# Optimization experiments

Measured on AMD Instinct MI355X. Metric: run time of the kernel, lower is better.

## Reference

```python
import math
import jax, jax.numpy as jnp
import numpy as np
from jax import lax

B = 8
IN_CH = 512
OUT_CH = 256
K = 3
LATENT = 512
BLUR = [1, 3, 3, 1]
FACTOR = 2
H = W = 64
# p = len(blur) - factor - (K-1) = 0 -> pad = ((p+1)//2 + factor - 1, p//2 + 1) = (1, 1)
PAD0, PAD1 = 1, 1


def _make_blur_kernel():
    k = jnp.array(BLUR, jnp.float32)
    k = k[None, :] * k[:, None]          # separable -> 2D
    k = k / jnp.sum(k)
    return k * (FACTOR ** 2)             # make_kernel(blur, factor) scales by factor^2


def setup_inputs() -> dict:
    key = jax.random.key(0)
    k1, k2, k3, k4 = jax.random.split(key, 4)
    inputs = {
        "input": jax.random.normal(k1, (B, IN_CH, H, W), jnp.float32),
        "w": jax.random.normal(k2, (B, LATENT), jnp.float32),
        # learned params
        "affine_weight": jax.random.normal(k3, (IN_CH, LATENT), jnp.float32),
        "affine_bias": jnp.ones((IN_CH,), jnp.float32),  # bias_init=1
        "conv_weight": jax.random.normal(k4, (1, OUT_CH, IN_CH, K, K), jnp.float32),
    }
    return inputs


def reference(input, w, affine_weight, affine_bias, conv_weight):
    batch = input.shape[0]
    # EqualLinear: scale = 1/sqrt(latent_dim), lr_mul=1
    style = w @ (affine_weight * (1.0 / math.sqrt(LATENT))).T + affine_bias  # (B, IN_CH)
    # modulate
    scale = 1.0 / math.sqrt(IN_CH * K * K)
    weight = (scale * conv_weight) * style[:, None, :, None, None]          # (B, OUT, IN, K, K)
    # demodulate over (in, kh, kw)
    demod = lax.rsqrt(jnp.sum(weight * weight, axis=(2, 3, 4)) + 1e-8)      # (B, OUT)
    weight = weight * demod[:, :, None, None, None]
    # grouped conv_transpose2d (groups=batch, stride=2, pad=0) == per-sample
    # conv with lhs_dilation=2, spatial padding K-1, kernel spatially flipped.
    kflip = jnp.flip(weight, (-2, -1))                                      # (B, OUT, IN, K, K) OIHW

    def ct(x, kern):  # x: (IN, H, W), kern: (OUT, IN, K, K)
        return lax.conv_general_dilated(
            x[None], kern, window_strides=(1, 1),
            padding=[(K - 1, K - 1), (K - 1, K - 1)],
            lhs_dilation=(2, 2),
            dimension_numbers=("NCHW", "OIHW", "NCHW"))[0]

    out = jax.vmap(ct)(input, kflip)                                        # (B, OUT, 2H-2+K, 2W-2+K)
    # upfirdn2d with up=down=1: pad then depthwise correlate with flipped FIR kernel
    blur = jnp.flip(_make_blur_kernel())                                    # (4, 4)
    out = jnp.pad(out, ((0, 0), (0, 0), (PAD0, PAD1), (PAD0, PAD1)))
    dw = jnp.tile(blur[None, None], (OUT_CH, 1, 1, 1))                      # (OUT, 1, 4, 4)
    out = lax.conv_general_dilated(
        out, dw, window_strides=(1, 1), padding="VALID",
        feature_group_count=OUT_CH,
        dimension_numbers=("NCHW", "OIHW", "NCHW"))
    return out  # (B, OUT, 2H, 2W)
```

## Files before the change

### kernel.cpp

```cpp
#include <hip/hip_runtime.h>
#include <hip/hip_bf16.h>
#include <math.h>

#define NB 8
#define INCH 512
#define OUTCH 256
#define SP 4096
#define LAT 512
#define NTAP 9
#define MDIM (NTAP*OUTCH)

#define INV_SQRT_LAT 0.044194173824159216f
#define WSCALE 0.014731391274719738f

typedef __bf16 bf16x8 __attribute__((ext_vector_type(8)));
typedef float  f32x4  __attribute__((ext_vector_type(4)));

__device__ __forceinline__ unsigned short f2bf(float f) {
  unsigned u = __float_as_uint(f);
  u += 0x7fffu + ((u >> 16) & 1u);
  return (unsigned short)(u >> 16);
}
__device__ __forceinline__ float bf2f(unsigned short v) {
  return __uint_as_float((unsigned)v << 16);
}

__global__ void prep_k(const float* __restrict__ w, const float* __restrict__ aff,
                       const float* __restrict__ bias, float* __restrict__ style,
                       const float* __restrict__ cw, float* __restrict__ S,
                       unsigned short* __restrict__ w9) {
  if (blockIdx.x < 16) {
    int gid = blockIdx.x * 256 + threadIdx.x;
    int b = gid >> 9, i = gid & 511;
    const float4* wv = (const float4*)(w + (size_t)b * LAT);
    const float4* av = (const float4*)(aff + (size_t)i * LAT);
    float s = 0.f;
#pragma unroll 4
    for (int l = 0; l < LAT / 4; ++l) {
      float4 a = av[l], ww = wv[l];
      s += a.x * ww.x + a.y * ww.y + a.z * ww.z + a.w * ww.w;
    }
    style[gid] = s * INV_SQRT_LAT + bias[i];
  } else {
    int gid = (blockIdx.x - 16) * 256 + threadIdx.x;
    int o = gid >> 9, i = gid & 511;
    const float* p = cw + (size_t)gid * 9;
    float ss = 0.f, v[9];
#pragma unroll
    for (int t = 0; t < 9; ++t) { v[t] = p[t]; ss += v[t] * v[t]; }
    S[gid] = ss * (WSCALE * WSCALE);
#pragma unroll
    for (int t = 0; t < 9; ++t)
      w9[((size_t)(t * OUTCH + o)) * INCH + i] = f2bf(v[t] * WSCALE);
  }
}

__global__ void demod_k(const float* __restrict__ style, const float* __restrict__ S,
                        float* __restrict__ dmod) {
  int gid = blockIdx.x * 256 + threadIdx.x;
  int b = gid >> 8, o = gid & 255;
  const float4* sv = (const float4*)(style + (size_t)b * INCH);
  const float4* Sv = (const float4*)(S + (size_t)o * INCH);
  float acc = 0.f;
#pragma unroll 4
  for (int l = 0; l < INCH / 4; ++l) {
    float4 st = sv[l], s2 = Sv[l];
    acc += st.x * st.x * s2.x + st.y * st.y * s2.y + st.z * st.z * s2.z + st.w * st.w * s2.w;
  }
  dmod[gid] = 1.0f / sqrtf(acc + 1e-8f);
}

__global__ void modx_k(const float* __restrict__ x, const float* __restrict__ style,
                       unsigned short* __restrict__ xmt) {
  __shared__ float tile[32][33];
  int b = blockIdx.z;
  int s0 = blockIdx.x * 32;
  int i0 = blockIdx.y * 32;
  int c = threadIdx.x & 31, r = threadIdx.x >> 5;
#pragma unroll
  for (int p = 0; p < 4; ++p) {
    int ii = r + p * 8;
    tile[ii][c] = x[((size_t)(b * INCH + i0 + ii)) * SP + s0 + c] * style[b * INCH + i0 + ii];
  }
  __syncthreads();
#pragma unroll
  for (int p = 0; p < 4; ++p) {
    int ss = r + p * 8;
    xmt[((size_t)(b * SP + s0 + ss)) * INCH + i0 + c] = f2bf(tile[c][ss]);
  }
}

__global__ __launch_bounds__(512, 2)
void gemm_k(const unsigned short* __restrict__ A,
            const unsigned short* __restrict__ Bm,
            unsigned short* __restrict__ C) {
  __shared__ __align__(16) unsigned short lds[73728];
  Bm += (size_t)blockIdx.z * SP * INCH;
  C  += (size_t)blockIdx.z * MDIM * SP;
  const int tid  = threadIdx.x;
  const int lane = tid & 63;
  const int wid  = tid >> 6;
  const int wm   = (wid >> 1) * 64;
  const int wn   = (wid & 1) * 64;
  const int m0 = blockIdx.y * 256;
  const int n0 = blockIdx.x * 128;
  const int r16  = lane & 15;
  const int quad = lane >> 4;

  const int srow = tid >> 3;
  const int sgch = ((tid & 7) ^ (srow & 7)) * 8;
  const int swb  = wid * 512;

  f32x4 acc[4][4];
#pragma unroll
  for (int i = 0; i < 4; ++i)
#pragma unroll
    for (int j = 0; j < 4; ++j) acc[i][j] = (f32x4){0.f, 0.f, 0.f, 0.f};

#define STAGE_A2(T, IT0) do {                                                       \
    unsigned short* _la = &lds[(((T) % 3) * 16384) + swb];                          \
    const unsigned short* _ga = A + (size_t)(m0 + srow) * INCH + (T) * 64 + sgch;   \
    _Pragma("unroll")                                                               \
    for (int _it = (IT0); _it < (IT0) + 2; ++_it)                                   \
      __builtin_amdgcn_global_load_lds(                                             \
          (const __attribute__((address_space(1))) void*)(_ga + (size_t)_it * 64 * INCH), \
          (__attribute__((address_space(3))) void*)(_la + _it * 4096), 16, 0, 0);   \
  } while (0)

#define STAGE_B1(T, IT) do {                                                        \
    unsigned short* _lb = &lds[49152 + (((T) % 3) * 8192) + swb];                   \
    const unsigned short* _gb = Bm + (size_t)(n0 + (IT) * 64 + srow) * INCH + (T) * 64 + sgch; \
    __builtin_amdgcn_global_load_lds(                                               \
        (const __attribute__((address_space(1))) void*)_gb,                         \
        (__attribute__((address_space(3))) void*)(_lb + (IT) * 4096), 16, 0, 0);    \
  } while (0)

#define READ_A(MH) do {                                                             \
    _Pragma("unroll")                                                               \
    for (int _i = 0; _i < 2; ++_i) {                                                \
      const int _ra = wm + ((MH) * 2 + _i) * 16 + r16;                              \
      af[0][_i] = *(const bf16x8*)&As_[_ra * 64 + (((0 + quad) ^ (_ra & 7)) * 8)];  \
      af[1][_i] = *(const bf16x8*)&As_[_ra * 64 + (((4 + quad) ^ (_ra & 7)) * 8)];  \
    }                                                                               \
  } while (0)

#define READ_B(NH) do {                                                             \
    _Pragma("unroll")                                                               \
    for (int _j = 0; _j < 2; ++_j) {                                                \
      const int _rb = wn + ((NH) * 2 + _j) * 16 + r16;                              \
      bfv[0][_j] = *(const bf16x8*)&Bs_[_rb * 64 + (((0 + quad) ^ (_rb & 7)) * 8)]; \
      bfv[1][_j] = *(const bf16x8*)&Bs_[_rb * 64 + (((4 + quad) ^ (_rb & 7)) * 8)]; \
    }                                                                               \
  } while (0)

#define MFMA_Q(MH, NH) do {                                                         \
    __builtin_amdgcn_s_setprio(1);                                                  \
    _Pragma("unroll")                                                               \
    for (int _kk = 0; _kk < 2; ++_kk)                                               \
    _Pragma("unroll")                                                               \
    for (int _i = 0; _i < 2; ++_i)                                                  \
    _Pragma("unroll")                                                               \
    for (int _j = 0; _j < 2; ++_j)                                                  \
      acc[(MH)*2+_i][(NH)*2+_j] = __builtin_amdgcn_mfma_f32_16x16x32_bf16(          \
          af[_kk][_i], bfv[_kk][_j], acc[(MH)*2+_i][(NH)*2+_j], 0, 0, 0);           \
    __builtin_amdgcn_s_setprio(0);                                                  \
  } while (0)

  STAGE_A2(0, 0); STAGE_A2(0, 2); STAGE_B1(0, 0); STAGE_B1(0, 1);
  STAGE_A2(1, 0); STAGE_A2(1, 2); STAGE_B1(1, 0); STAGE_B1(1, 1);
  asm volatile("s_waitcnt vmcnt(6)" ::: "memory");
  __builtin_amdgcn_sched_barrier(0);
  __builtin_amdgcn_s_barrier();

  for (int t = 0; t < 8; ++t) {
    const unsigned short* As_ = &lds[(t % 3) * 16384];
    const unsigned short* Bs_ = &lds[49152 + (t % 3) * 8192];
    const bool st = (t < 6);
    bf16x8 af[2][2], bfv[2][2];
    if (st) STAGE_A2(t + 2, 0);
    READ_A(0); READ_B(0);
    __builtin_amdgcn_s_barrier();
    MFMA_Q(0, 0);
    __builtin_amdgcn_s_barrier();
    if (st) STAGE_A2(t + 2, 2);
    READ_B(1);
    __builtin_amdgcn_s_barrier();
    MFMA_Q(0, 1);
    __builtin_amdgcn_s_barrier();
    if (st) STAGE_B1(t + 2, 0);
    READ_A(1);
    __builtin_amdgcn_s_barrier();
    MFMA_Q(1, 1);
    __builtin_amdgcn_s_barrier();
    if (st) STAGE_B1(t + 2, 1);
    READ_B(0);
    __builtin_amdgcn_s_barrier();
    MFMA_Q(1, 0);
    if (t < 6) {
      asm volatile("s_waitcnt vmcnt(6)" ::: "memory");
      __builtin_amdgcn_sched_barrier(0);
    } else if (t == 6) {
      asm volatile("s_waitcnt vmcnt(0)" ::: "memory");
      __builtin_amdgcn_sched_barrier(0);
    }
    __builtin_amdgcn_s_barrier();
  }
#undef STAGE_A2
#undef STAGE_B1
#undef READ_A
#undef READ_B
#undef MFMA_Q

#pragma unroll
  for (int i = 0; i < 4; ++i)
#pragma unroll
    for (int j = 0; j < 4; ++j)
#pragma unroll
      for (int r = 0; r < 4; ++r) {
        int row = wm + i * 16 + quad * 4 + r;
        int col = wn + j * 16 + r16;
        int pc  = (col >> 3) ^ (row & 15);
        lds[row * 128 + pc * 8 + (col & 7)] = f2bf(acc[i][j][r]);
      }
  __syncthreads();
#pragma unroll
  for (int rr = 0; rr < 8; ++rr) {
    int row = rr * 32 + (tid >> 4);
    int c   = tid & 15;
    int pc  = c ^ (row & 15);
    uint4 v = *(const uint4*)&lds[row * 128 + pc * 8];
    *(uint4*)&C[(size_t)(m0 + row) * SP + n0 + c * 8] = v;
  }
}

#define STRIP 8
#define TLSTR 70
#define TLROWS 10
__global__ __launch_bounds__(256)
void combine_k(const unsigned short* __restrict__ T, const float* __restrict__ dm,
               float* __restrict__ out) {
  __shared__ __align__(16) unsigned short TlB[9 * TLROWS * TLSTR + 4];
  __shared__ __align__(16) float V[3 * TLROWS * 128];
  T   += (size_t)blockIdx.z * MDIM * SP;
  dm  += (size_t)blockIdx.z * OUTCH;
  out += (size_t)blockIdx.z * OUTCH * 128 * 128;
  const int o  = blockIdx.y;
  const int Y0 = blockIdx.x * STRIP;
  const int tid = threadIdx.x;

  {
    uint4* tz = (uint4*)TlB;
#pragma unroll
    for (int idx = tid; idx < 788; idx += 256) tz[idx] = (uint4){0u, 0u, 0u, 0u};
  }
  __syncthreads();

  for (int idx = tid; idx < 1440; idx += 256) {
    int tap = idx / 160;
    int rem = idx - tap * 160;
    int ry  = rem >> 4;
    int c16 = rem & 15;
    int Yg = Y0 - 1 + ry;
    if ((unsigned)Yg < 64u) {
      ushort4 v4 = *(const ushort4*)(T + (size_t)(tap * OUTCH + o) * SP + Yg * 64 + c16 * 4);
      unsigned short* dst = &TlB[(tap * TLROWS + ry) * TLSTR + 4 + c16 * 4];
      *(ushort2*)(dst)     = make_ushort2(v4.x, v4.y);
      *(ushort2*)(dst + 2) = make_ushort2(v4.z, v4.w);
    }
  }
  __syncthreads();

  {
    const int r  = tid >> 3;
    const int xc = tid & 7;
    if (r < 30) {
      const int c  = r / 10;
      const int yr = r - c * 10;
      const int X0 = xc * 8;
      float td[3][12];
#pragma unroll
      for (int d = 0; d < 3; ++d) {
        const unsigned short* src = &TlB[((c * 3 + d) * TLROWS + yr) * TLSTR + 2 + X0];
#pragma unroll
        for (int k = 0; k < 6; ++k) {
          ushort2 u2 = *(const ushort2*)(src + 2 * k);
          td[d][2 * k]     = bf2f(u2.x);
          td[d][2 * k + 1] = bf2f(u2.y);
        }
      }
      float vout[16];
#pragma unroll
      for (int Xl = 0; Xl < 8; ++Xl) {
        float a0 = td[0][Xl + 1], a1 = td[0][Xl + 2], a2 = td[0][Xl + 3];
        float b0 = td[1][Xl + 1], b1 = td[1][Xl + 2], b2 = td[1][Xl + 3];
        float c0 = td[2][Xl + 1], c1 = td[2][Xl + 2], c2 = td[2][Xl + 3];
        vout[2 * Xl]     = b0 + 3.f * c0 + 3.f * a1 + 3.f * b1 + c1 + a2;
        vout[2 * Xl + 1] = c0 + a1 + 3.f * b1 + 3.f * c1 + 3.f * a2 + b2;
      }
      float* vr = &V[(c * TLROWS + yr) * 128];
#pragma unroll
      for (int j = 0; j < 4; ++j) {
        int l = 4 * xc + j;
        int p = (l & ~3) | ((l & 3) ^ ((l >> 3) & 3));
        *(f32x4*)(vr + p * 4) = (f32x4){vout[4 * j], vout[4 * j + 1], vout[4 * j + 2], vout[4 * j + 3]};
      }
    }
  }
  __syncthreads();

  {
    const int y  = tid >> 4;
    const int py = y & 1;
    const int Yl = y >> 1;
    const float dmv = dm[o] * (1.0f / 16.0f);
    float* orow = out + ((size_t)o * 128 + (Y0 * 2 + y)) * 128;
#pragma unroll
    for (int xg = 0; xg < 2; ++xg) {
      int l = (tid & 15) + 16 * xg;
      int p = (l & ~3) | ((l & 3) ^ ((l >> 3) & 3));
      int off = p * 4;
      f32x4 v00 = *(const f32x4*)&V[((0 * TLROWS) + Yl + 0) * 128 + off];
      f32x4 v01 = *(const f32x4*)&V[((0 * TLROWS) + Yl + 1) * 128 + off];
      f32x4 v02 = *(const f32x4*)&V[((0 * TLROWS) + Yl + 2) * 128 + off];
      f32x4 v10 = *(const f32x4*)&V[((1 * TLROWS) + Yl + 0) * 128 + off];
      f32x4 v11 = *(const f32x4*)&V[((1 * TLROWS) + Yl + 1) * 128 + off];
      f32x4 v12 = *(const f32x4*)&V[((1 * TLROWS) + Yl + 2) * 128 + off];
      f32x4 v20 = *(const f32x4*)&V[((2 * TLROWS) + Yl + 0) * 128 + off];
      f32x4 v21 = *(const f32x4*)&V[((2 * TLROWS) + Yl + 1) * 128 + off];
      f32x4 v22 = *(const f32x4*)&V[((2 * TLROWS) + Yl + 2) * 128 + off];
      f32x4 r;
      if (py == 0)
        r = v10 + 3.f * v20 + 3.f * v01 + 3.f * v11 + v21 + v02;
      else
        r = v20 + v01 + 3.f * v11 + 3.f * v21 + 3.f * v02 + v12;
      r *= dmv;
      *(f32x4*)(orow + l * 4) = r;
    }
  }
}

extern "C" void kernel_launch(void* const* d_in, const int* in_sizes, int n_in,
                              void* d_out, int out_size, void* d_ws, size_t ws_size,
                              hipStream_t stream) {
  const float* x    = (const float*)d_in[0];
  const float* w    = (const float*)d_in[1];
  const float* aff  = (const float*)d_in[2];
  const float* bias = (const float*)d_in[3];
  const float* cw   = (const float*)d_in[4];
  float* out = (float*)d_out;
  char* ws = (char*)d_ws;
  float* style        = (float*)(ws);
  float* S            = (float*)(ws + 16384);
  float* dmod         = (float*)(ws + 540672);
  unsigned short* w9  = (unsigned short*)(ws + 548864);
  unsigned short* xmt = (unsigned short*)(ws + 2908160);
  unsigned short* T   = (unsigned short*)(ws + 36462592);

  hipLaunchKernelGGL(prep_k, dim3(528), dim3(256), 0, stream, w, aff, bias, style, cw, S, w9);
  hipLaunchKernelGGL(demod_k, dim3(8), dim3(256), 0, stream, style, S, dmod);
  hipLaunchKernelGGL(modx_k, dim3(128, 16, 8), dim3(256), 0, stream, x, style, xmt);
  hipLaunchKernelGGL(gemm_k, dim3(32, 9, NB), dim3(512), 0, stream, w9, xmt, T);
  hipLaunchKernelGGL(combine_k, dim3(64 / STRIP, 256, NB), dim3(256), 0, stream, T, dmod, out);
}
```

Measured before the change: 396.4 us.

## Parallelize demod reduction, vectorize modx stores, and double combine strip height

The demod kernel now gives each (batch, out-channel) pair 16 threads that reduce with shuffles, so the launch grows from 8 blocks to 128 and no longer leaves most of the GPU idle. The transposed bf16 stores in modx are grouped into 8-byte ushort4 writes instead of scalar 2-byte writes. The combine kernel handles 16 rows per block instead of 8, which lowers halo reloads and block count. The cost is more LDS per combine block, which could reduce occupancy.

After: 385.2 us. 2.8% less time.

```diff
diff --git a/kernel.cpp b/kernel.cpp
--- a/kernel.cpp
+++ b/kernel.cpp
@@ -57,17 +57,20 @@
 
 __global__ void demod_k(const float* __restrict__ style, const float* __restrict__ S,
                         float* __restrict__ dmod) {
-  int gid = blockIdx.x * 256 + threadIdx.x;
-  int b = gid >> 8, o = gid & 255;
-  const float4* sv = (const float4*)(style + (size_t)b * INCH);
-  const float4* Sv = (const float4*)(S + (size_t)o * INCH);
+  int g = blockIdx.x * 16 + (threadIdx.x >> 4);
+  int j = threadIdx.x & 15;
+  int b = g >> 8, o = g & 255;
+  const float4* sv = (const float4*)(style + (size_t)b * INCH + j * 32);
+  const float4* Sv = (const float4*)(S + (size_t)o * INCH + j * 32);
   float acc = 0.f;
-#pragma unroll 4
-  for (int l = 0; l < INCH / 4; ++l) {
+#pragma unroll
+  for (int l = 0; l < 8; ++l) {
     float4 st = sv[l], s2 = Sv[l];
     acc += st.x * st.x * s2.x + st.y * st.y * s2.y + st.z * st.z * s2.z + st.w * st.w * s2.w;
   }
-  dmod[gid] = 1.0f / sqrtf(acc + 1e-8f);
+#pragma unroll
+  for (int d = 1; d < 16; d <<= 1) acc += __shfl_xor(acc, d, 16);
+  if (j == 0) dmod[g] = 1.0f / sqrtf(acc + 1e-8f);
 }
 
 __global__ void modx_k(const float* __restrict__ x, const float* __restrict__ style,
@@ -83,10 +86,15 @@
     tile[ii][c] = x[((size_t)(b * INCH + i0 + ii)) * SP + s0 + c] * style[b * INCH + i0 + ii];
   }
   __syncthreads();
-#pragma unroll
-  for (int p = 0; p < 4; ++p) {
-    int ss = r + p * 8;
-    xmt[((size_t)(b * SP + s0 + ss)) * INCH + i0 + c] = f2bf(tile[c][ss]);
+  {
+    int ss = threadIdx.x >> 3;
+    int c4 = threadIdx.x & 7;
+    ushort4 v;
+    v.x = f2bf(tile[c4 * 4 + 0][ss]);
+    v.y = f2bf(tile[c4 * 4 + 1][ss]);
+    v.z = f2bf(tile[c4 * 4 + 2][ss]);
+    v.w = f2bf(tile[c4 * 4 + 3][ss]);
+    *(ushort4*)&xmt[((size_t)(b * SP + s0 + ss)) * INCH + i0 + c4 * 4] = v;
   }
 }
 
@@ -233,9 +241,9 @@
   }
 }
 
-#define STRIP 8
+#define STRIP 16
 #define TLSTR 70
-#define TLROWS 10
+#define TLROWS 18
 __global__ __launch_bounds__(256)
 void combine_k(const unsigned short* __restrict__ T, const float* __restrict__ dm,
                float* __restrict__ out) {
@@ -250,76 +258,77 @@
 
   {
     uint4* tz = (uint4*)TlB;
-#pragma unroll
-    for (int idx = tid; idx < 788; idx += 256) tz[idx] = (uint4){0u, 0u, 0u, 0u};
-  }
-  __syncthreads();
-
-  for (int idx = tid; idx < 1440; idx += 256) {
-    int tap = idx / 160;
-    int rem = idx - tap * 160;
-    int ry  = rem >> 4;
-    int c16 = rem & 15;
-    int Yg = Y0 - 1 + ry;
+    for (int idx = tid; idx < (9 * TLROWS * TLSTR + 4) / 8; idx += 256)
+      tz[idx] = (uint4){0u, 0u, 0u, 0u};
+  }
+  __syncthreads();
+
+  for (int idx = tid; idx < 9 * TLROWS * 8; idx += 256) {
+    int tap = idx / (TLROWS * 8);
+    int rem = idx - tap * (TLROWS * 8);
+    int ry  = rem >> 3;
+    int c8  = rem & 7;
+    int Yg  = Y0 - 1 + ry;
     if ((unsigned)Yg < 64u) {
-      ushort4 v4 = *(const ushort4*)(T + (size_t)(tap * OUTCH + o) * SP + Yg * 64 + c16 * 4);
-      unsigned short* dst = &TlB[(tap * TLROWS + ry) * TLSTR + 4 + c16 * 4];
-      *(ushort2*)(dst)     = make_ushort2(v4.x, v4.y);
-      *(ushort2*)(dst + 2) = make_ushort2(v4.z, v4.w);
+      const unsigned short* src = T + (size_t)(tap * OUTCH + o) * SP + Yg * 64 + c8 * 8;
+      ushort4 a  = *(const ushort4*)(src);
+      ushort4 b4 = *(const ushort4*)(src + 4);
+      unsigned short* dst = &TlB[(tap * TLROWS + ry) * TLSTR + 4 + c8 * 8];
+      *(ushort2*)(dst)     = make_ushort2(a.x, a.y);
+      *(ushort2*)(dst + 2) = make_ushort2(a.z, a.w);
+      *(ushort2*)(dst + 4) = make_ushort2(b4.x, b4.y);
+      *(ushort2*)(dst + 6) = make_ushort2(b4.z, b4.w);
+    }
+  }
+  __syncthreads();
+
+  for (int idx = tid; idx < 3 * TLROWS * 8; idx += 256) {
+    const int r  = idx >> 3;
+    const int xc = idx & 7;
+    const int c  = r / TLROWS;
+    const int yr = r - c * TLROWS;
+    const int X0 = xc * 8;
+    float td[3][12];
+#pragma unroll
+    for (int d = 0; d < 3; ++d) {
+      const unsigned short* src = &TlB[((c * 3 + d) * TLROWS + yr) * TLSTR + 2 + X0];
+#pragma unroll
+      for (int k = 0; k < 6; ++k) {
+        ushort2 u2 = *(const ushort2*)(src + 2 * k);
+        td[d][2 * k]     = bf2f(u2.x);
+        td[d][2 * k + 1] = bf2f(u2.y);
+      }
+    }
+    float vout[16];
+#pragma unroll
+    for (int Xl = 0; Xl < 8; ++Xl) {
+      float a0 = td[0][Xl + 1], a1 = td[0][Xl + 2], a2 = td[0][Xl + 3];
+      float b0 = td[1][Xl + 1], b1 = td[1][Xl + 2], b2 = td[1][Xl + 3];
+      float c0 = td[2][Xl + 1], c1 = td[2][Xl + 2], c2 = td[2][Xl + 3];
+      vout[2 * Xl]     = b0 + 3.f * c0 + 3.f * a1 + 3.f * b1 + c1 + a2;
+      vout[2 * Xl + 1] = c0 + a1 + 3.f * b1 + 3.f * c1 + 3.f * a2 + b2;
+    }
+    float* vr = &V[(c * TLROWS + yr) * 128];
+#pragma unroll
+    for (int j = 0; j < 4; ++j) {
+      int l = 4 * xc + j;
+      int p = (l & ~3) | ((l & 3) ^ ((l >> 3) & 3));
+      *(f32x4*)(vr + p * 4) = (f32x4){vout[4 * j], vout[4 * j + 1], vout[4 * j + 2], vout[4 * j + 3]};
     }
   }
   __syncthreads();
 
   {
-    const int r  = tid >> 3;
-    const int xc = tid & 7;
-    if (r < 30) {
-      const int c  = r / 10;
-      const int yr = r - c * 10;
-      const int X0 = xc * 8;
-      float td[3][12];
-#pragma unroll
-      for (int d = 0; d < 3; ++d) {
-        const unsigned short* src = &TlB[((c * 3 + d) * TLROWS + yr) * TLSTR + 2 + X0];
-#pragma unroll
-        for (int k = 0; k < 6; ++k) {
-          ushort2 u2 = *(const ushort2*)(src + 2 * k);
-          td[d][2 * k]     = bf2f(u2.x);
-          td[d][2 * k + 1] = bf2f(u2.y);
-        }
-      }
-      float vout[16];
-#pragma unroll
-      for (int Xl = 0; Xl < 8; ++Xl) {
-        float a0 = td[0][Xl + 1], a1 = td[0][Xl + 2], a2 = td[0][Xl + 3];
-        float b0 = td[1][Xl + 1], b1 = td[1][Xl + 2], b2 = td[1][Xl + 3];
-        float c0 = td[2][Xl + 1], c1 = td[2][Xl + 2], c2 = td[2][Xl + 3];
-        vout[2 * Xl]     = b0 + 3.f * c0 + 3.f * a1 + 3.f * b1 + c1 + a2;
-        vout[2 * Xl + 1] = c0 + a1 + 3.f * b1 + 3.f * c1 + 3.f * a2 + b2;
-      }
-      float* vr = &V[(c * TLROWS + yr) * 128];
-#pragma unroll
-      for (int j = 0; j < 4; ++j) {
-        int l = 4 * xc + j;
-        int p = (l & ~3) | ((l & 3) ^ ((l >> 3) & 3));
-        *(f32x4*)(vr + p * 4) = (f32x4){vout[4 * j], vout[4 * j + 1], vout[4 * j + 2], vout[4 * j + 3]};
-      }
-    }
-  }
-  __syncthreads();
-
-  {
-    const int y  = tid >> 4;
+    const int y  = tid >> 3;
     const int py = y & 1;
     const int Yl = y >> 1;
     const float dmv = dm[o] * (1.0f / 16.0f);
     float* orow = out + ((size_t)o * 128 + (Y0 * 2 + y)) * 128;
 #pragma unroll
-    for (int xg = 0; xg < 2; ++xg) {
-      int l = (tid & 15) + 16 * xg;
+    for (int xg = 0; xg < 4; ++xg) {
+      int l = (tid & 7) + 8 * xg;
       int p = (l & ~3) | ((l & 3) ^ ((l >> 3) & 3));
       int off = p * 4;
-      f32x4 v00 = *(const f32x4*)&V[((0 * TLROWS) + Yl + 0) * 128 + off];
       f32x4 v01 = *(const f32x4*)&V[((0 * TLROWS) + Yl + 1) * 128 + off];
       f32x4 v02 = *(const f32x4*)&V[((0 * TLROWS) + Yl + 2) * 128 + off];
       f32x4 v10 = *(const f32x4*)&V[((1 * TLROWS) + Yl + 0) * 128 + off];
@@ -357,7 +366,7 @@
   unsigned short* T   = (unsigned short*)(ws + 36462592);
 
   hipLaunchKernelGGL(prep_k, dim3(528), dim3(256), 0, stream, w, aff, bias, style, cw, S, w9);
-  hipLaunchKernelGGL(demod_k, dim3(8), dim3(256), 0, stream, style, S, dmod);
+  hipLaunchKernelGGL(demod_k, dim3(128), dim3(256), 0, stream, style, S, dmod);
   hipLaunchKernelGGL(modx_k, dim3(128, 16, 8), dim3(256), 0, stream, x, style, xmt);
   hipLaunchKernelGGL(gemm_k, dim3(32, 9, NB), dim3(512), 0, stream, w9, xmt, T);
   hipLaunchKernelGGL(combine_k, dim3(64 / STRIP, 256, NB), dim3(256), 0, stream, T, dmod, out);
```
